# Optimization experiments

Hardware: AMD Instinct MI355X
Metric: run time of the kernel (lower is better)

## Reference

```python
import jax, jax.numpy as jnp
import numpy as np

N_HEADS = 16
WINDOW = 256  # window_size; keep keys with |i-j| <= WINDOW//2


def setup_inputs() -> dict:
    key = jax.random.key(0)
    ks = jax.random.split(key, 6)
    B, S, D = 2, 2048, 1024
    x = jax.random.normal(ks[0], (B, S, D), dtype=jnp.float32)
    # torch nn.Linear weights are [out_features, in_features]
    scale = 1.0 / np.sqrt(D)
    Wq = jax.random.normal(ks[1], (D, D), dtype=jnp.float32) * scale
    Wk = jax.random.normal(ks[2], (D, D), dtype=jnp.float32) * scale
    Wv = jax.random.normal(ks[3], (D, D), dtype=jnp.float32) * scale
    Wo = jax.random.normal(ks[4], (D, D), dtype=jnp.float32) * scale
    # standard ALiBi slopes: 2^(-8*(h+1)/H)
    slopes = jnp.asarray(2.0 ** (-8.0 * (np.arange(1, N_HEADS + 1) / N_HEADS)), dtype=jnp.float32)
    return {"x": x, "Wq": Wq, "Wk": Wk, "Wv": Wv, "Wo": Wo, "slopes": slopes}


def reference(x, Wq, Wk, Wv, Wo, slopes):
    B, S, D = x.shape
    H = N_HEADS
    dk = D // H
    # projections (torch Linear: y = x @ W.T)
    q = jnp.einsum('bsd,od->bso', x, Wq).reshape(B, S, H, dk)
    k = jnp.einsum('bsd,od->bso', x, Wk).reshape(B, S, H, dk)
    v = jnp.einsum('bsd,od->bso', x, Wv).reshape(B, S, H, dk)
    # full score matrix [B,H,S,S]
    scores = jnp.einsum('bqhd,bkhd->bhqk', q, k) / jnp.sqrt(jnp.asarray(dk, x.dtype))
    pos = jnp.arange(S)
    rel = (pos[:, None] - pos[None, :]).astype(x.dtype)          # [S,S] q_pos - k_pos
    scores = scores + slopes[None, :, None, None] * rel[None, None]
    window_mask = jnp.abs(pos[:, None] - pos[None, :]) <= (WINDOW // 2)  # [S,S]
    scores = jnp.where(window_mask[None, None], scores, -jnp.inf)
    attn = jax.nn.softmax(scores, axis=-1)
    out = jnp.einsum('bhqk,bkhd->bqhd', attn, v).reshape(B, S, D)
    return jnp.einsum('bsd,od->bso', out, Wo)
```

## Files before the change

kernel.cpp:

```cpp
#include <hip/hip_runtime.h>
#include <hip/hip_bf16.h>

#define S_LEN   2048
#define D_MODEL 1024
#define NH      16
#define DK      64
#define BATCH   2
#define M_ROWS  (BATCH * S_LEN)
#define LDP     72
#define LDV     66
#define LDW     132

typedef __attribute__((ext_vector_type(8))) short bf16x8;
typedef __attribute__((ext_vector_type(4))) float f32x4;
typedef __attribute__((ext_vector_type(16))) float f32x16;
typedef __attribute__((ext_vector_type(8))) unsigned short us8;
typedef __attribute__((ext_vector_type(4))) unsigned short us4;

static __device__ __forceinline__ unsigned short f2bf(float f) {
    unsigned u = __builtin_bit_cast(unsigned, f);
    u += 0x7fffu + ((u >> 16) & 1u);
    return (unsigned short)(u >> 16);
}

__global__ __launch_bounds__(256) void cvt_all(const float* __restrict__ x,
                                               const float* __restrict__ wq,
                                               const float* __restrict__ wk,
                                               const float* __restrict__ wv,
                                               const float* __restrict__ wo,
                                               unsigned short* __restrict__ dst) {
    const int b = blockIdx.x;
    if (b < 2048) {
        const size_t o8 = (size_t)b * 256 + threadIdx.x;
        const float4* s = (const float4*)x + o8 * 2;
        float4 a = s[0], bb = s[1];
        us8 o;
        o[0] = f2bf(a.x);  o[1] = f2bf(a.y);  o[2] = f2bf(a.z);  o[3] = f2bf(a.w);
        o[4] = f2bf(bb.x); o[5] = f2bf(bb.y); o[6] = f2bf(bb.z); o[7] = f2bf(bb.w);
        *((us8*)dst + o8) = o;
    } else {
        const int wi = (b - 2048) >> 9;
        const float* src = (wi == 0) ? wq : (wi == 1) ? wk : (wi == 2) ? wv : wo;
        const size_t local = (size_t)((b - 2048) & 511) * 256 + threadIdx.x;
        const float4* s = (const float4*)src + local * 2;
        float4 a = s[0], bb = s[1];
        us8 o;
        o[0] = f2bf(a.x);  o[1] = f2bf(a.y);  o[2] = f2bf(a.z);  o[3] = f2bf(a.w);
        o[4] = f2bf(bb.x); o[5] = f2bf(bb.y); o[6] = f2bf(bb.z); o[7] = f2bf(bb.w);
        *((us8*)dst + 524288 + (size_t)wi * 131072 + local) = o;
    }
}

template <int STORE_BF16, int BN>
__global__ __launch_bounds__(256) void mfma_gemm_bt(const unsigned short* __restrict__ A,
                                                    const unsigned short* __restrict__ W,
                                                    void* __restrict__ Cv, int N) {
    constexpr int K = 1024, BM = 128, BK = 64;
    constexpr int MI = (BN == 128) ? 2 : 1;
    constexpr int SMEM = (STORE_BF16 && BN == 128) ? (128 * LDW)
                                                   : (BM * BK + BN * BK);
    __shared__ unsigned short smem[SMEM];
    unsigned short* As = smem;
    unsigned short* Bs = smem + BM * BK;

    const int tid  = threadIdx.x;
    const int w    = tid >> 6;
    const int lane = tid & 63;
    const int m0 = blockIdx.y * BM;
    const int n0 = blockIdx.x * BN;
    const int wr = (BN == 128) ? (w >> 1) * 64 : w * 32;
    const int wc = (BN == 128) ? (w & 1) * 64 : 0;

    const int srow   = lane >> 3;
    const int schunk = ((lane & 7) ^ (lane >> 3)) * 8;
    const int l31   = lane & 31;
    const int khalf = lane >> 5;
    const int sw    = lane & 7;
    int roff[4];
#pragma unroll
    for (int s = 0; s < 4; ++s)
        roff[s] = ((2 * s + khalf) ^ sw) * 8;

    f32x16 acc[MI][2] = {};

    for (int k0 = 0; k0 < K; k0 += BK) {
        __syncthreads();
#pragma unroll
        for (int t = 0; t < 4; ++t) {
            const int rbase = w * 32 + t * 8;
            const unsigned short* ga = A + (size_t)(m0 + rbase + srow) * K + k0 + schunk;
            __builtin_amdgcn_global_load_lds(
                (const __attribute__((address_space(1))) void*)ga,
                (__attribute__((address_space(3))) void*)(As + rbase * BK), 16, 0, 0);
        }
#pragma unroll
        for (int t = 0; t < BN / 32; ++t) {
            const int rbase = w * (BN / 4) + t * 8;
            const unsigned short* gb = W + (size_t)(n0 + rbase + srow) * K + k0 + schunk;
            __builtin_amdgcn_global_load_lds(
                (const __attribute__((address_space(1))) void*)gb,
                (__attribute__((address_space(3))) void*)(Bs + rbase * BK), 16, 0, 0);
        }
        __syncthreads();

#pragma unroll
        for (int s = 0; s < 4; ++s) {
            bf16x8 af[MI], bfr[2];
#pragma unroll
            for (int i = 0; i < MI; ++i)
                af[i] = *(const bf16x8*)(As + (wr + i * 32 + l31) * BK + roff[s]);
#pragma unroll
            for (int j = 0; j < 2; ++j)
                bfr[j] = *(const bf16x8*)(Bs + (wc + j * 32 + l31) * BK + roff[s]);
#pragma unroll
            for (int i = 0; i < MI; ++i)
#pragma unroll
                for (int j = 0; j < 2; ++j)
                    acc[i][j] = __builtin_amdgcn_mfma_f32_32x32x16_bf16(af[i], bfr[j], acc[i][j], 0, 0, 0);
        }
    }

    if constexpr (STORE_BF16 && BN == 128) {
        __syncthreads();
#pragma unroll
        for (int i = 0; i < 2; ++i)
#pragma unroll
            for (int j = 0; j < 2; ++j)
#pragma unroll
                for (int r = 0; r < 16; ++r) {
                    const int row_l = wr + i * 32 + (r & 3) + 8 * (r >> 2) + 4 * khalf;
                    const int col_l = wc + j * 32 + l31;
                    smem[row_l * LDW + col_l] = f2bf(acc[i][j][r]);
                }
        __syncthreads();
#pragma unroll
        for (int e = 0; e < 8; ++e) {
            const int idx = e * 256 + tid;
            const int row = idx >> 4;
            const int cc  = (idx & 15) * 8;
            us4 lo = *(const us4*)(smem + row * LDW + cc);
            us4 hi = *(const us4*)(smem + row * LDW + cc + 4);
            us8 v;
            v[0] = lo[0]; v[1] = lo[1]; v[2] = lo[2]; v[3] = lo[3];
            v[4] = hi[0]; v[5] = hi[1]; v[6] = hi[2]; v[7] = hi[3];
            *(us8*)((unsigned short*)Cv + (size_t)(m0 + row) * N + n0 + cc) = v;
        }
    } else {
#pragma unroll
        for (int i = 0; i < MI; ++i)
#pragma unroll
            for (int j = 0; j < 2; ++j)
#pragma unroll
                for (int r = 0; r < 16; ++r) {
                    const int gm = m0 + wr + i * 32 + (r & 3) + 8 * (r >> 2) + 4 * khalf;
                    const int gn = n0 + wc + j * 32 + l31;
                    if (STORE_BF16)
                        ((unsigned short*)Cv)[(size_t)gm * N + gn] = f2bf(acc[i][j][r]);
                    else
                        ((float*)Cv)[(size_t)gm * N + gn] = acc[i][j][r];
                }
    }
}

__global__ __launch_bounds__(256) void attn_mfma(const unsigned short* __restrict__ qkvb,
                                                 const float* __restrict__ slopes,
                                                 unsigned short* __restrict__ aoutb) {
    __shared__ unsigned short QPs[64 * LDP];
    __shared__ unsigned short Ks[2 * 64 * 64];
    __shared__ unsigned short Vt[64 * LDV];

    const int tid  = threadIdx.x;
    const int w    = tid >> 6;
    const int lane = tid & 63;
    const int q0 = blockIdx.x * 64;
    const int h  = blockIdx.y;
    const int b  = blockIdx.z;
    const float slope = slopes[h];
    const size_t rowbase = (size_t)b * S_LEN * 3072;

#pragma unroll
    for (int e = 0; e < 2; ++e) {
        int idx = e * 256 + tid;
        int r = idx >> 3, cc = (idx & 7) * 8;
        us8 v = *(const us8*)(qkvb + rowbase + (size_t)(q0 + r) * 3072 + h * DK + cc);
        *(us8*)(QPs + r * LDP + cc) = v;
    }

    const int col = lane & 15;
    const int rq  = (lane >> 4) * 4;
    const int wq  = w * 16;
    const int fo  = (lane >> 4) * 8;

    const int srowK   = lane >> 3;
    const int schunkK = ((lane & 7) ^ srowK) * 8;
    const int kc0 = (((lane >> 4) + 0) ^ (lane & 7)) * 8;
    const int kc1 = (((lane >> 4) + 4) ^ (lane & 7)) * 8;

    const unsigned short* kbase  = qkvb + rowbase + 1024 + h * DK;
    const unsigned short* vbase0 = qkvb + rowbase + 2048 + h * DK;

    const int rp  = tid >> 3;
    const int ccv = (tid & 7) * 8;

    float qa[4];
#pragma unroll
    for (int r = 0; r < 4; ++r) {
        const int qpos = q0 + wq + rq + r;
        qa[r] = slope * (float)(qpos > 128 ? qpos - 128 : 0) - 12.0f;
    }

    f32x4 o_acc[4] = {};
    float l_part[4] = {0.f, 0.f, 0.f, 0.f};

    {
        const int k0 = q0 - 128;
#pragma unroll
        for (int t = 0; t < 2; ++t) {
            const int rbase = w * 16 + t * 8;
            const unsigned short* gk = kbase + (long long)(k0 + rbase + srowK) * 3072 + schunkK;
            __builtin_amdgcn_global_load_lds(
                (const __attribute__((address_space(1))) void*)gk,
                (__attribute__((address_space(3))) void*)(Ks + rbase * 64), 16, 0, 0);
        }
        const long long kp0 = (long long)(k0 + rp * 2);
        us8 v0 = *(const us8*)(vbase0 + ccv + kp0 * 3072);
        us8 v1 = *(const us8*)(vbase0 + ccv + (kp0 + 1) * 3072);
#pragma unroll
        for (int t = 0; t < 8; ++t) {
            unsigned pk = (unsigned)(unsigned short)v0[t] | ((unsigned)(unsigned short)v1[t] << 16);
            *(unsigned*)(Vt + (ccv + t) * LDV + rp * 2) = pk;
        }
    }
    __syncthreads();

    const bf16x8 aq0 = *(const bf16x8*)(QPs + (wq + col) * LDP + fo);
    const bf16x8 aq1 = *(const bf16x8*)(QPs + (wq + col) * LDP + fo + 32);

    int cur = 0;
    for (int c = 0; c < 5; ++c) {
        const int k0 = q0 - 128 + c * 64;
        const unsigned short* KsC = Ks + cur * 4096;
        const bool have_next = (c < 4);

        us8 nv0, nv1;
        if (have_next) {
            const int kn0 = k0 + 64;
            unsigned short* KsN = (unsigned short*)Ks + (cur ^ 1) * 4096;
#pragma unroll
            for (int t = 0; t < 2; ++t) {
                const int rbase = w * 16 + t * 8;
                const unsigned short* gk = kbase + (long long)(kn0 + rbase + srowK) * 3072 + schunkK;
                __builtin_amdgcn_global_load_lds(
                    (const __attribute__((address_space(1))) void*)gk,
                    (__attribute__((address_space(3))) void*)(KsN + rbase * 64), 16, 0, 0);
            }
            const long long kp0 = (long long)(kn0 + rp * 2);
            nv0 = *(const us8*)(vbase0 + ccv + kp0 * 3072);
            nv1 = *(const us8*)(vbase0 + ccv + (kp0 + 1) * 3072);
        }

        f32x4 sacc[4] = {};
        __builtin_amdgcn_s_setprio(1);
#pragma unroll
        for (int j = 0; j < 4; ++j) {
            const int tt  = wq - 64 * c - 16 * j;
            const int klo = k0 + 16 * j;
            const bool any_v = (tt <= 0) && (tt >= -256) && (klo < S_LEN) && (klo + 15 >= 0);
            if (any_v) {
                bf16x8 bk0 = *(const bf16x8*)(KsC + (j * 16 + col) * 64 + kc0);
                bf16x8 bk1 = *(const bf16x8*)(KsC + (j * 16 + col) * 64 + kc1);
                sacc[j] = __builtin_amdgcn_mfma_f32_16x16x32_bf16(aq0, bk0, sacc[j], 0, 0, 0);
                sacc[j] = __builtin_amdgcn_mfma_f32_16x16x32_bf16(aq1, bk1, sacc[j], 0, 0, 0);
            }
        }
        __builtin_amdgcn_s_setprio(0);

#pragma unroll
        for (int j = 0; j < 4; ++j) {
            const int tt  = wq - 64 * c - 16 * j;
            const int klo = k0 + 16 * j;
            const bool any_v = (tt <= 0) && (tt >= -256) && (klo < S_LEN) && (klo + 15 >= 0);
            unsigned short* ps = QPs + (wq + rq) * LDP + j * 16 + col;
            if (!any_v) {
#pragma unroll
                for (int r = 0; r < 4; ++r) ps[r * LDP] = 0;
            } else {
                const float kb = slope * (float)(klo + col);
                const bool all_v = (tt <= -16) && (tt >= -240) && (klo >= 0) && (klo + 15 < S_LEN);
                if (all_v) {
#pragma unroll
                    for (int r = 0; r < 4; ++r) {
                        float p = __expf(fmaf(sacc[j][r], 0.125f, qa[r] - kb));
                        l_part[r] += p;
                        ps[r * LDP] = f2bf(p);
                    }
                } else {
                    const int kpos = klo + col;
                    const bool kin = (unsigned)kpos < (unsigned)S_LEN;
#pragma unroll
                    for (int r = 0; r < 4; ++r) {
                        const int rel = (q0 + wq + rq + r) - kpos;
                        const bool ok = kin && (rel <= 128) && (rel >= -128);
                        float p = 0.f;
                        if (ok) p = __expf(fmaf(sacc[j][r], 0.125f, qa[r] - kb));
                        l_part[r] += p;
                        ps[r * LDP] = f2bf(p);
                    }
                }
            }
        }

        {
            bf16x8 ap0 = *(const bf16x8*)(QPs + (wq + col) * LDP + fo);
            bf16x8 ap1 = *(const bf16x8*)(QPs + (wq + col) * LDP + fo + 32);
            __builtin_amdgcn_s_setprio(1);
#pragma unroll
            for (int j = 0; j < 4; ++j) {
                bf16x8 bv0 = *(const bf16x8*)(Vt + (j * 16 + col) * LDV + fo);
                bf16x8 bv1 = *(const bf16x8*)(Vt + (j * 16 + col) * LDV + fo + 32);
                o_acc[j] = __builtin_amdgcn_mfma_f32_16x16x32_bf16(ap0, bv0, o_acc[j], 0, 0, 0);
                o_acc[j] = __builtin_amdgcn_mfma_f32_16x16x32_bf16(ap1, bv1, o_acc[j], 0, 0, 0);
            }
            __builtin_amdgcn_s_setprio(0);
        }

        if (have_next) {
            __syncthreads();
#pragma unroll
            for (int t = 0; t < 8; ++t) {
                unsigned pk = (unsigned)(unsigned short)nv0[t] | ((unsigned)(unsigned short)nv1[t] << 16);
                *(unsigned*)(Vt + (ccv + t) * LDV + rp * 2) = pk;
            }
            __syncthreads();
        }
        cur ^= 1;
    }

    float inv[4];
#pragma unroll
    for (int r = 0; r < 4; ++r) {
        float l = l_part[r];
#pragma unroll
        for (int off = 1; off < 16; off <<= 1) l += __shfl_xor(l, off, 64);
        inv[r] = 1.f / l;
    }

#pragma unroll
    for (int j = 0; j < 4; ++j)
#pragma unroll
        for (int r = 0; r < 4; ++r) {
            const int qpos = q0 + wq + rq + r;
            aoutb[((size_t)b * S_LEN + qpos) * D_MODEL + h * DK + j * 16 + col] =
                f2bf(o_acc[j][r] * inv[r]);
        }
}

extern "C" void kernel_launch(void* const* d_in, const int* in_sizes, int n_in,
                              void* d_out, int out_size, void* d_ws, size_t ws_size,
                              hipStream_t stream) {
    const float* x      = (const float*)d_in[0];
    const float* Wq     = (const float*)d_in[1];
    const float* Wk     = (const float*)d_in[2];
    const float* Wv     = (const float*)d_in[3];
    const float* Wo     = (const float*)d_in[4];
    const float* slopes = (const float*)d_in[5];
    float* out = (float*)d_out;

    unsigned short* xb    = (unsigned short*)d_ws;
    unsigned short* wb    = xb    + (size_t)M_ROWS * D_MODEL;
    unsigned short* wob   = wb    + (size_t)3072 * D_MODEL;
    unsigned short* qkvb  = wob   + (size_t)1024 * D_MODEL;
    unsigned short* aoutb = qkvb  + (size_t)M_ROWS * 3072;

    dim3 blk(256);
    cvt_all<<<4096, blk, 0, stream>>>(x, Wq, Wk, Wv, Wo, xb);
    mfma_gemm_bt<1, 128><<<dim3(3072 / 128, M_ROWS / 128), blk, 0, stream>>>(xb, wb, qkvb, 3072);
    attn_mfma<<<dim3(S_LEN / 64, NH, BATCH), blk, 0, stream>>>(qkvb, slopes, aoutb);
    mfma_gemm_bt<0, 128><<<dim3(1024 / 128, M_ROWS / 128), blk, 0, stream>>>(aoutb, wob, out, 1024);
}
```

Baseline: 156.4 us.

## Add dedicated output-projection GEMM with 128x64 tiles and double-panel LDS loads

Replaces the generic templated GEMM for the final Wo projection with a specialized kernel that uses 128x64 output tiles. This doubles the grid from 256 to 512 blocks to fill more CUs on the MI355X. It loads two K-panels per sync via global_load_lds with XOR-swizzled LDS addressing. The trade-off is less reuse per block, more redundant A-tile traffic, and a compute phase that does not overlap the loads.

Measured after the change: 154.8 us. About the same (-1.0%).

```diff
diff --git a/kernel.cpp b/kernel.cpp
--- a/kernel.cpp
+++ b/kernel.cpp
@@ -162,6 +162,100 @@
     }
 }
 
+__global__ __launch_bounds__(256) void gemm_wo(const unsigned short* __restrict__ A,
+                                               const unsigned short* __restrict__ W,
+                                               float* __restrict__ C) {
+    constexpr int K = 1024, BM = 128, BN = 64, BK = 64;
+    constexpr int PANEL = BM * BK + BN * BK;
+    __shared__ unsigned short smem[2 * PANEL];
+    unsigned short* As0 = smem;
+    unsigned short* Bs0 = smem + BM * BK;
+    unsigned short* As1 = smem + PANEL;
+    unsigned short* Bs1 = smem + PANEL + BM * BK;
+
+    const int tid  = threadIdx.x;
+    const int w    = tid >> 6;
+    const int lane = tid & 63;
+    const int m0 = blockIdx.y * BM;
+    const int n0 = blockIdx.x * BN;
+    const int wr = w * 32;
+
+    const int srow   = lane >> 3;
+    const int schunk = ((lane & 7) ^ (lane >> 3)) * 8;
+    const int l31   = lane & 31;
+    const int khalf = lane >> 5;
+    const int sw    = lane & 7;
+    int roff[4];
+#pragma unroll
+    for (int s = 0; s < 4; ++s)
+        roff[s] = ((2 * s + khalf) ^ sw) * 8;
+
+    f32x16 acc[2] = {};
+
+    for (int k0 = 0; k0 < K; k0 += 2 * BK) {
+        __syncthreads();
+#pragma unroll
+        for (int t = 0; t < 4; ++t) {
+            const int rbase = w * 32 + t * 8;
+            const unsigned short* ga = A + (size_t)(m0 + rbase + srow) * K + k0 + schunk;
+            __builtin_amdgcn_global_load_lds(
+                (const __attribute__((address_space(1))) void*)ga,
+                (__attribute__((address_space(3))) void*)(As0 + rbase * BK), 16, 0, 0);
+        }
+#pragma unroll
+        for (int t = 0; t < 2; ++t) {
+            const int rbase = w * 16 + t * 8;
+            const unsigned short* gb = W + (size_t)(n0 + rbase + srow) * K + k0 + schunk;
+            __builtin_amdgcn_global_load_lds(
+                (const __attribute__((address_space(1))) void*)gb,
+                (__attribute__((address_space(3))) void*)(Bs0 + rbase * BK), 16, 0, 0);
+        }
+#pragma unroll
+        for (int t = 0; t < 4; ++t) {
+            const int rbase = w * 32 + t * 8;
+            const unsigned short* ga = A + (size_t)(m0 + rbase + srow) * K + k0 + BK + schunk;
+            __builtin_amdgcn_global_load_lds(
+                (const __attribute__((address_space(1))) void*)ga,
+                (__attribute__((address_space(3))) void*)(As1 + rbase * BK), 16, 0, 0);
+        }
+#pragma unroll
+        for (int t = 0; t < 2; ++t) {
+            const int rbase = w * 16 + t * 8;
+            const unsigned short* gb = W + (size_t)(n0 + rbase + srow) * K + k0 + BK + schunk;
+            __builtin_amdgcn_global_load_lds(
+                (const __attribute__((address_space(1))) void*)gb,
+                (__attribute__((address_space(3))) void*)(Bs1 + rbase * BK), 16, 0, 0);
+        }
+        __syncthreads();
+
+#pragma unroll
+        for (int s = 0; s < 4; ++s) {
+            bf16x8 af = *(const bf16x8*)(As0 + (wr + l31) * BK + roff[s]);
+            bf16x8 b0 = *(const bf16x8*)(Bs0 + (l31) * BK + roff[s]);
+            bf16x8 b1 = *(const bf16x8*)(Bs0 + (32 + l31) * BK + roff[s]);
+            acc[0] = __builtin_amdgcn_mfma_f32_32x32x16_bf16(af, b0, acc[0], 0, 0, 0);
+            acc[1] = __builtin_amdgcn_mfma_f32_32x32x16_bf16(af, b1, acc[1], 0, 0, 0);
+        }
+#pragma unroll
+        for (int s = 0; s < 4; ++s) {
+            bf16x8 af = *(const bf16x8*)(As1 + (wr + l31) * BK + roff[s]);
+            bf16x8 b0 = *(const bf16x8*)(Bs1 + (l31) * BK + roff[s]);
+            bf16x8 b1 = *(const bf16x8*)(Bs1 + (32 + l31) * BK + roff[s]);
+            acc[0] = __builtin_amdgcn_mfma_f32_32x32x16_bf16(af, b0, acc[0], 0, 0, 0);
+            acc[1] = __builtin_amdgcn_mfma_f32_32x32x16_bf16(af, b1, acc[1], 0, 0, 0);
+        }
+    }
+
+#pragma unroll
+    for (int j = 0; j < 2; ++j)
+#pragma unroll
+        for (int r = 0; r < 16; ++r) {
+            const int gm = m0 + wr + (r & 3) + 8 * (r >> 2) + 4 * khalf;
+            const int gn = n0 + j * 32 + l31;
+            C[(size_t)gm * 1024 + gn] = acc[j][r];
+        }
+}
+
 __global__ __launch_bounds__(256) void attn_mfma(const unsigned short* __restrict__ qkvb,
                                                  const float* __restrict__ slopes,
                                                  unsigned short* __restrict__ aoutb) {
@@ -376,5 +470,5 @@
     cvt_all<<<4096, blk, 0, stream>>>(x, Wq, Wk, Wv, Wo, xb);
     mfma_gemm_bt<1, 128><<<dim3(3072 / 128, M_ROWS / 128), blk, 0, stream>>>(xb, wb, qkvb, 3072);
     attn_mfma<<<dim3(S_LEN / 64, NH, BATCH), blk, 0, stream>>>(qkvb, slopes, aoutb);
-    mfma_gemm_bt<0, 128><<<dim3(1024 / 128, M_ROWS / 128), blk, 0, stream>>>(aoutb, wob, out, 1024);
-}
+    gemm_wo<<<dim3(1024 / 64, M_ROWS / 128), blk, 0, stream>>>(aoutb, wob, out);
+}
```
